# Kernel tuning notes

Hardware: AMD Instinct MI355X
Metric: run time of the kernel (lower is better)

Reference implementation:

```python
import jax, jax.numpy as jnp
import numpy as np


def setup_inputs() -> dict:
    key = jax.random.key(0)
    ks = jax.random.split(key, 7)
    B = 65536
    x = jax.random.normal(ks[0], (B, 1, 28, 28), dtype=jnp.float32)
    conv_w = jax.random.normal(ks[1], (4, 1, 7, 7), dtype=jnp.float32) * 0.1
    conv_b = jax.random.normal(ks[2], (4,), dtype=jnp.float32) * 0.1
    fc1_w = jax.random.normal(ks[3], (64, 256), dtype=jnp.float32) * 0.05
    fc1_b = jax.random.normal(ks[4], (64,), dtype=jnp.float32) * 0.05
    fc2_w = jax.random.normal(ks[5], (10, 64), dtype=jnp.float32) * 0.1
    fc2_b = jax.random.normal(ks[6], (10,), dtype=jnp.float32) * 0.1
    return {"x": x, "conv_w": conv_w, "conv_b": conv_b,
            "fc1_w": fc1_w, "fc1_b": fc1_b, "fc2_w": fc2_w, "fc2_b": fc2_b}


def reference(x, conv_w, conv_b, fc1_w, fc1_b, fc2_w, fc2_b):
    # conv1: 1->4 channels, 7x7 kernel, stride 3, no padding -> [B,4,8,8]
    h = jax.lax.conv_general_dilated(
        x, conv_w, window_strides=(3, 3), padding="VALID",
        dimension_numbers=("NCHW", "OIHW", "NCHW"))
    h = h + conv_b[None, :, None, None]
    h = h * h  # SquareFunction (CKKS polynomial activation)
    h = h.reshape(h.shape[0], -1)  # [B, 256]
    h = jnp.einsum("bi,oi->bo", h, fc1_w) + fc1_b
    h = h * h  # SquareFunction
    out = jnp.einsum("bi,oi->bo", h, fc2_w) + fc2_b  # [B, 10]
    return out
```

## Files before the change

kernel.cpp:

```cpp
#include <hip/hip_runtime.h>


#define BLK_IMGS    32
#define CHUNK_IMGS  4
#define NCHUNK      8
#define XCH_FLOATS  (CHUNK_IMGS * 784)
#define HB_PITCH    33
#define H2_PITCH    33

#define LDS_XBUF    0
#define LDS_H       3136
#define LDS_W2      11584
#define LDS_TOTAL_F 12608

__global__ __launch_bounds__(512)
void encconv_fused9(const float* __restrict__ x,
                    const float* __restrict__ conv_w,
                    const float* __restrict__ conv_b,
                    const float* __restrict__ fc1_w,
                    const float* __restrict__ fc1_b,
                    const float* __restrict__ fc2_w,
                    const float* __restrict__ fc2_b,
                    float* __restrict__ out)
{
    extern __shared__ float lds[];
    float*  xbuf = lds + LDS_XBUF;
    float*  hbf  = lds + LDS_H;
    float4* hb   = (float4*)hbf;
    float4* h2b  = (float4*)(lds + LDS_XBUF);
    float*  ob   = lds + LDS_XBUF + 2112;
    float4* w2b  = (float4*)(lds + LDS_W2);

    const int tid  = threadIdx.x;
    const int blk  = blockIdx.x;
    const long base_img = (long)blk * BLK_IMGS;

    const int lane = tid & 63;
    const int wv   = tid >> 6;

    const int c    = __builtin_amdgcn_readfirstlane(wv >> 1);
    const int gh   = __builtin_amdgcn_readfirstlane(wv & 1);
    const int gl   = lane >> 5;
    const int y    = (lane >> 2) & 7;
    const int xq   = lane & 3;
    const int g    = gh * 2 + gl;
    const int x0   = xq & 1;
    const int xh2  = xq >> 1;

    float ws[49];
    #pragma unroll
    for (int i = 0; i < 49; ++i) ws[i] = conv_w[c * 49 + i];
    const float cb = conv_b[c];

    if (tid < 160) {
        float4 v = *(const float4*)(fc2_w + tid * 4);
        int e  = tid * 4;
        int j  = e >> 6;
        int kk = (e & 63) >> 2;
        w2b[kk * 16 + j] = v;
    }

    const float* xblk = x + base_img * 784;

    float4 pf0, pf1;
    {
        pf0 = *(const float4*)(xblk + 4 * tid);
        if (tid < 272) pf1 = *(const float4*)(xblk + 4 * (tid + 512));
    }

    for (int ch = 0; ch < NCHUNK; ++ch) {
        *(float4*)(xbuf + 4 * tid) = pf0;
        if (tid < 272) *(float4*)(xbuf + 4 * (tid + 512)) = pf1;
        __syncthreads();

        if (ch + 1 < NCHUNK) {
            const float* src = xblk + (ch + 1) * XCH_FLOATS;
            pf0 = *(const float4*)(src + 4 * tid);
            if (tid < 272) pf1 = *(const float4*)(src + 4 * (tid + 512));
        }

        float acc0 = 0.f, acc1 = 0.f;
        const float* xi = xbuf + g * 784;
        #pragma unroll
        for (int rr = 0; rr < 7; ++rr) {
            const float* rp = xi + (3 * y + rr) * 28 + 6 * xq;
            float2 q0 = *(const float2*)(rp + 0);
            float2 q1 = *(const float2*)(rp + 2);
            float2 q2 = *(const float2*)(rp + 4);
            float2 q3 = *(const float2*)(rp + 6);
            float2 q4 = *(const float2*)(rp + 8);
            float r[10] = { q0.x, q0.y, q1.x, q1.y, q2.x,
                            q2.y, q3.x, q3.y, q4.x, q4.y };
            #pragma unroll
            for (int kx = 0; kx < 7; ++kx) {
                const float w = ws[rr * 7 + kx];
                acc0 = fmaf(r[0 + kx], w, acc0);
                acc1 = fmaf(r[3 + kx], w, acc1);
            }
        }

        float h0 = acc0 + cb; h0 *= h0;
        float h1 = acc1 + cb; h1 *= h1;
        const int k4  = c * 16 + y * 2 + xh2;
        const int img = ch * CHUNK_IMGS + g;
        float2 hv2; hv2.x = h0; hv2.y = h1;
        *(float2*)(hbf + (k4 * HB_PITCH + img) * 4 + 2 * x0) = hv2;

        __syncthreads();
    }

    {
        const int img = lane & 31;
        const int oh  = lane >> 5;
        const int w8  = __builtin_amdgcn_readfirstlane(wv);
        const float* wbase = fc1_w + (w8 * 8) * 256;

        float a0=0.f,a1=0.f,a2=0.f,a3=0.f,a4=0.f,a5=0.f,a6=0.f,a7=0.f;

        #pragma unroll 2
        for (int k4 = 0; k4 < 64; ++k4) {
            float4 h4 = hb[k4 * HB_PITCH + img];
            const float* wp = wbase + k4 * 4;
            float4 w0 = *(const float4*)(wp + 0 * 256);
            float4 w1 = *(const float4*)(wp + 1 * 256);
            float4 w2 = *(const float4*)(wp + 2 * 256);
            float4 w3 = *(const float4*)(wp + 3 * 256);
            float4 w4 = *(const float4*)(wp + 4 * 256);
            float4 w5 = *(const float4*)(wp + 5 * 256);
            float4 w6 = *(const float4*)(wp + 6 * 256);
            float4 w7 = *(const float4*)(wp + 7 * 256);
            a0 = fmaf(h4.x,w0.x,a0); a0 = fmaf(h4.y,w0.y,a0); a0 = fmaf(h4.z,w0.z,a0); a0 = fmaf(h4.w,w0.w,a0);
            a1 = fmaf(h4.x,w1.x,a1); a1 = fmaf(h4.y,w1.y,a1); a1 = fmaf(h4.z,w1.z,a1); a1 = fmaf(h4.w,w1.w,a1);
            a2 = fmaf(h4.x,w2.x,a2); a2 = fmaf(h4.y,w2.y,a2); a2 = fmaf(h4.z,w2.z,a2); a2 = fmaf(h4.w,w2.w,a2);
            a3 = fmaf(h4.x,w3.x,a3); a3 = fmaf(h4.y,w3.y,a3); a3 = fmaf(h4.z,w3.z,a3); a3 = fmaf(h4.w,w3.w,a3);
            a4 = fmaf(h4.x,w4.x,a4); a4 = fmaf(h4.y,w4.y,a4); a4 = fmaf(h4.z,w4.z,a4); a4 = fmaf(h4.w,w4.w,a4);
            a5 = fmaf(h4.x,w5.x,a5); a5 = fmaf(h4.y,w5.y,a5); a5 = fmaf(h4.z,w5.z,a5); a5 = fmaf(h4.w,w5.w,a5);
            a6 = fmaf(h4.x,w6.x,a6); a6 = fmaf(h4.y,w6.y,a6); a6 = fmaf(h4.z,w6.z,a6); a6 = fmaf(h4.w,w6.w,a6);
            a7 = fmaf(h4.x,w7.x,a7); a7 = fmaf(h4.y,w7.y,a7); a7 = fmaf(h4.z,w7.z,a7); a7 = fmaf(h4.w,w7.w,a7);
        }

        const float* bp = fc1_b + w8 * 8;
        float s0 = oh ? a4 : a0;  float b0 = oh ? bp[4] : bp[0];
        float s1 = oh ? a5 : a1;  float b1 = oh ? bp[5] : bp[1];
        float s2 = oh ? a6 : a2;  float b2 = oh ? bp[6] : bp[2];
        float s3 = oh ? a7 : a3;  float b3 = oh ? bp[7] : bp[3];
        float4 p0;
        p0.x = s0 + b0; p0.x *= p0.x;
        p0.y = s1 + b1; p0.y *= p0.y;
        p0.z = s2 + b2; p0.z *= p0.z;
        p0.w = s3 + b3; p0.w *= p0.w;
        h2b[(w8 * 2 + oh) * H2_PITCH + img] = p0;
    }
    __syncthreads();

    {
        const int im5 = tid >> 4;
        const int q   = tid & 15;
        if (q < 10) {
            float s = 0.f;
            #pragma unroll
            for (int k4 = 0; k4 < 16; ++k4) {
                float4 hh = h2b[k4 * H2_PITCH + im5];
                float4 wA = w2b[k4 * 16 + q];
                s = fmaf(hh.x, wA.x, s); s = fmaf(hh.y, wA.y, s);
                s = fmaf(hh.z, wA.z, s); s = fmaf(hh.w, wA.w, s);
            }
            ob[im5 * 10 + q] = s + fc2_b[q];
        }
    }
    __syncthreads();

    if (tid < 80) {
        float4 v = *(const float4*)(ob + tid * 4);
        *(float4*)(out + (long)blk * 320 + tid * 4) = v;
    }
}

extern "C" void kernel_launch(void* const* d_in, const int* in_sizes, int n_in,
                              void* d_out, int out_size, void* d_ws, size_t ws_size,
                              hipStream_t stream) {
    const float* x      = (const float*)d_in[0];
    const float* conv_w = (const float*)d_in[1];
    const float* conv_b = (const float*)d_in[2];
    const float* fc1_w  = (const float*)d_in[3];
    const float* fc1_b  = (const float*)d_in[4];
    const float* fc2_w  = (const float*)d_in[5];
    const float* fc2_b  = (const float*)d_in[6];
    float* out = (float*)d_out;

    const int B = in_sizes[0] / 784;
    const int blocks = (B + BLK_IMGS - 1) / BLK_IMGS;
    const size_t lds_bytes = LDS_TOTAL_F * sizeof(float);

    encconv_fused9<<<blocks, 512, lds_bytes, stream>>>(
        x, conv_w, conv_b, fc1_w, fc1_b, fc2_w, fc2_b, out);
}
```

Measured before the change: 334.2 us.

## Compute conv directly from global memory with per-thread register tiling

Replaces the chunked LDS staging of input images (with per-chunk barriers and register prefetch) by having each thread load its image's rows directly from global memory and compute a 2x8 output tile in registers, reusing loaded rows across two output rows. This removes LDS traffic and many __syncthreads for the conv stage and shrinks LDS usage. It risks uncoalesced strided global loads across lanes and higher register pressure.

```diff
diff --git a/kernel.cpp b/kernel.cpp
--- a/kernel.cpp
+++ b/kernel.cpp
@@ -2,34 +2,30 @@
 
 
 #define BLK_IMGS    32
-#define CHUNK_IMGS  4
-#define NCHUNK      8
-#define XCH_FLOATS  (CHUNK_IMGS * 784)
 #define HB_PITCH    33
 #define H2_PITCH    33
 
-#define LDS_XBUF    0
-#define LDS_H       3136
-#define LDS_W2      11584
-#define LDS_TOTAL_F 12608
+#define LDS_H       0
+#define LDS_H2      8448
+#define LDS_W2      10560
+#define LDS_OUT     11584
+#define LDS_TOTAL_F 11904
 
 __global__ __launch_bounds__(512)
-void encconv_fused9(const float* __restrict__ x,
-                    const float* __restrict__ conv_w,
-                    const float* __restrict__ conv_b,
-                    const float* __restrict__ fc1_w,
-                    const float* __restrict__ fc1_b,
-                    const float* __restrict__ fc2_w,
-                    const float* __restrict__ fc2_b,
-                    float* __restrict__ out)
+void encconv_fused10(const float* __restrict__ x,
+                     const float* __restrict__ conv_w,
+                     const float* __restrict__ conv_b,
+                     const float* __restrict__ fc1_w,
+                     const float* __restrict__ fc1_b,
+                     const float* __restrict__ fc2_w,
+                     const float* __restrict__ fc2_b,
+                     float* __restrict__ out)
 {
     extern __shared__ float lds[];
-    float*  xbuf = lds + LDS_XBUF;
-    float*  hbf  = lds + LDS_H;
-    float4* hb   = (float4*)hbf;
-    float4* h2b  = (float4*)(lds + LDS_XBUF);
-    float*  ob   = lds + LDS_XBUF + 2112;
-    float4* w2b  = (float4*)(lds + LDS_W2);
+    float4* hb  = (float4*)(lds + LDS_H);
+    float4* h2b = (float4*)(lds + LDS_H2);
+    float4* w2b = (float4*)(lds + LDS_W2);
+    float*  ob  = lds + LDS_OUT;
 
     const int tid  = threadIdx.x;
     const int blk  = blockIdx.x;
@@ -38,14 +34,11 @@
     const int lane = tid & 63;
     const int wv   = tid >> 6;
 
-    const int c    = __builtin_amdgcn_readfirstlane(wv >> 1);
-    const int gh   = __builtin_amdgcn_readfirstlane(wv & 1);
-    const int gl   = lane >> 5;
-    const int y    = (lane >> 2) & 7;
-    const int xq   = lane & 3;
-    const int g    = gh * 2 + gl;
-    const int x0   = xq & 1;
-    const int xh2  = xq >> 1;
+    const int c   = __builtin_amdgcn_readfirstlane(wv >> 1);
+    const int yph = __builtin_amdgcn_readfirstlane(wv & 1);
+    const int ypl = lane >> 5;
+    const int yp  = yph * 2 + ypl;
+    const int g   = lane & 31;
 
     float ws[49];
     #pragma unroll
@@ -60,54 +53,60 @@
         w2b[kk * 16 + j] = v;
     }
 
-    const float* xblk = x + base_img * 784;
+    float accA[8], accB[8];
+    #pragma unroll
+    for (int i = 0; i < 8; ++i) { accA[i] = 0.f; accB[i] = 0.f; }
 
-    float4 pf0, pf1;
-    {
-        pf0 = *(const float4*)(xblk + 4 * tid);
-        if (tid < 272) pf1 = *(const float4*)(xblk + 4 * (tid + 512));
+    const float* xi = x + (base_img + g) * 784 + yp * 6 * 28;
+    #pragma unroll
+    for (int wrow = 0; wrow < 10; ++wrow) {
+        const float* rp = xi + wrow * 28;
+        float4 r0 = *(const float4*)(rp + 0);
+        float4 r1 = *(const float4*)(rp + 4);
+        float4 r2 = *(const float4*)(rp + 8);
+        float4 r3 = *(const float4*)(rp + 12);
+        float4 r4 = *(const float4*)(rp + 16);
+        float4 r5 = *(const float4*)(rp + 20);
+        float4 r6 = *(const float4*)(rp + 24);
+        float r[28] = { r0.x,r0.y,r0.z,r0.w, r1.x,r1.y,r1.z,r1.w,
+                        r2.x,r2.y,r2.z,r2.w, r3.x,r3.y,r3.z,r3.w,
+                        r4.x,r4.y,r4.z,r4.w, r5.x,r5.y,r5.z,r5.w,
+                        r6.x,r6.y,r6.z,r6.w };
+        if (wrow <= 6) {
+            #pragma unroll
+            for (int kx = 0; kx < 7; ++kx) {
+                const float wA = ws[wrow * 7 + kx];
+                #pragma unroll
+                for (int col = 0; col < 8; ++col)
+                    accA[col] = fmaf(r[3 * col + kx], wA, accA[col]);
+            }
+        }
+        if (wrow >= 3) {
+            #pragma unroll
+            for (int kx = 0; kx < 7; ++kx) {
+                const float wB = ws[(wrow - 3) * 7 + kx];
+                #pragma unroll
+                for (int col = 0; col < 8; ++col)
+                    accB[col] = fmaf(r[3 * col + kx], wB, accB[col]);
+            }
+        }
     }
 
-    for (int ch = 0; ch < NCHUNK; ++ch) {
-        *(float4*)(xbuf + 4 * tid) = pf0;
-        if (tid < 272) *(float4*)(xbuf + 4 * (tid + 512)) = pf1;
-        __syncthreads();
-
-        if (ch + 1 < NCHUNK) {
-            const float* src = xblk + (ch + 1) * XCH_FLOATS;
-            pf0 = *(const float4*)(src + 4 * tid);
-            if (tid < 272) pf1 = *(const float4*)(src + 4 * (tid + 512));
+    #pragma unroll
+    for (int ty = 0; ty < 2; ++ty) {
+        const float* a = ty ? accB : accA;
+        const int y = 2 * yp + ty;
+        #pragma unroll
+        for (int xh = 0; xh < 2; ++xh) {
+            float4 hv;
+            hv.x = a[4 * xh + 0] + cb; hv.x *= hv.x;
+            hv.y = a[4 * xh + 1] + cb; hv.y *= hv.y;
+            hv.z = a[4 * xh + 2] + cb; hv.z *= hv.z;
+            hv.w = a[4 * xh + 3] + cb; hv.w *= hv.w;
+            hb[(c * 16 + y * 2 + xh) * HB_PITCH + g] = hv;
         }
-
-        float acc0 = 0.f, acc1 = 0.f;
-        const float* xi = xbuf + g * 784;
-        #pragma unroll
-        for (int rr = 0; rr < 7; ++rr) {
-            const float* rp = xi + (3 * y + rr) * 28 + 6 * xq;
-            float2 q0 = *(const float2*)(rp + 0);
-            float2 q1 = *(const float2*)(rp + 2);
-            float2 q2 = *(const float2*)(rp + 4);
-            float2 q3 = *(const float2*)(rp + 6);
-            float2 q4 = *(const float2*)(rp + 8);
-            float r[10] = { q0.x, q0.y, q1.x, q1.y, q2.x,
-                            q2.y, q3.x, q3.y, q4.x, q4.y };
-            #pragma unroll
-            for (int kx = 0; kx < 7; ++kx) {
-                const float w = ws[rr * 7 + kx];
-                acc0 = fmaf(r[0 + kx], w, acc0);
-                acc1 = fmaf(r[3 + kx], w, acc1);
-            }
-        }
-
-        float h0 = acc0 + cb; h0 *= h0;
-        float h1 = acc1 + cb; h1 *= h1;
-        const int k4  = c * 16 + y * 2 + xh2;
-        const int img = ch * CHUNK_IMGS + g;
-        float2 hv2; hv2.x = h0; hv2.y = h1;
-        *(float2*)(hbf + (k4 * HB_PITCH + img) * 4 + 2 * x0) = hv2;
-
-        __syncthreads();
     }
+    __syncthreads();
 
     {
         const int img = lane & 31;
@@ -192,6 +191,6 @@
     const int blocks = (B + BLK_IMGS - 1) / BLK_IMGS;
     const size_t lds_bytes = LDS_TOTAL_F * sizeof(float);
 
-    encconv_fused9<<<blocks, 512, lds_bytes, stream>>>(
+    encconv_fused10<<<blocks, 512, lds_bytes, stream>>>(
         x, conv_w, conv_b, fc1_w, fc1_b, fc2_w, fc2_b, out);
 }
```

New measurement: 485.0 us. +45.1%, slower.
